# Kernel optimization log

Measured on AMD Instinct MI355X. Metric: run time of the kernel, lower is better.

## Reference

```python
import jax, jax.numpy as jnp
import numpy as np
from functools import partial

N = 10  # n_qubits (static)


def _rx(state, w, theta, n):
    # state: [B, 2^n] complex64; RX(theta) on wire w (wire 0 = most significant)
    B = state.shape[0]
    st = state.reshape(B, 2 ** w, 2, 2 ** (n - 1 - w))
    half = jnp.asarray(theta, state.real.dtype) * 0.5
    c = jnp.cos(half).reshape(-1, 1, 1)
    s = jnp.sin(half).reshape(-1, 1, 1)
    s0, s1 = st[:, :, 0], st[:, :, 1]
    n0 = c * s0 - 1j * s * s1
    n1 = -1j * s * s0 + c * s1
    return jnp.stack([n0, n1], axis=2).reshape(B, 2 ** n)


def _cnot(state, control, target, n):
    B = state.shape[0]
    a, bb = (control, target) if control < target else (target, control)
    st = state.reshape(B, 2 ** a, 2, 2 ** (bb - a - 1), 2, 2 ** (n - 1 - bb))
    if control == a:
        # control is axis 2, target axis 4: flip target where control==1
        c1 = jnp.flip(st[:, :, 1], axis=3)
        st = jnp.stack([st[:, :, 0], c1], axis=2)
    else:
        # control is axis 4, target axis 2: flip axis-2 slice where control==1
        c1 = jnp.flip(st[:, :, :, :, 1], axis=1)
        st = jnp.stack([st[:, :, :, :, 0], c1], axis=4)
    return st.reshape(B, 2 ** n)


def _expect_z(state, n):
    B = state.shape[0]
    probs = jnp.abs(state) ** 2  # [B, 2^n]
    es = []
    for w in range(n):
        p = probs.reshape(B, 2 ** w, 2, 2 ** (n - 1 - w))
        es.append(p[:, :, 0].sum((1, 2)) - p[:, :, 1].sum((1, 2)))
    return jnp.stack(es, axis=1)  # [B, n]


def _qlayer(x, theta, n):
    # x: [B, n] encoder angles; theta: [n] trainable RX angles
    B = x.shape[0]
    state = jnp.zeros((B, 2 ** n), jnp.complex64).at[:, 0].set(1.0)
    for w in range(n):
        state = _rx(state, w, x[:, w], n)
    for w in range(n):
        state = _rx(state, w, theta[w], n)
    for w in range(n - 1):
        state = _cnot(state, w, w + 1, n)
    state = _cnot(state, n - 1, 0, n)
    return _expect_z(state, n)


def setup_inputs() -> dict:
    key = jax.random.key(0)
    k1, k2, k3, k4 = jax.random.split(key, 4)
    T, B, D, H = 64, 256, 246, N
    inputs = jax.random.normal(k1, (T, B, D), jnp.float32)
    fan_in = D + H
    W = jax.random.normal(k2, (4, N, fan_in), jnp.float32) / np.sqrt(fan_in)
    b = jax.random.normal(k3, (4, N), jnp.float32) * 0.01
    thetas = jax.random.normal(k4, (4, N), jnp.float32)
    return {"inputs": inputs, "W": W, "b": b, "thetas": thetas}


def reference(inputs, W, b, thetas):
    T, B, D = inputs.shape
    H = thetas.shape[-1]
    qlayer4 = jax.vmap(partial(_qlayer, n=N))  # over the 4 gates

    def step(carry, x_t):
        hx, cx = carry
        comb = jnp.concatenate([x_t, hx], axis=1)          # [B, D+H]
        z = jnp.einsum('bi,goi->gbo', comb, W) + b[:, None, :]  # [4, B, n]
        gates = qlayer4(z, thetas)                          # [4, B, n]
        f = jax.nn.sigmoid(gates[0])
        i = jax.nn.sigmoid(gates[1])
        g = jnp.tanh(gates[2])
        o = jax.nn.sigmoid(gates[3])
        cx = f * cx + i * g
        hx = o * jnp.tanh(cx)
        return (hx, cx), hx

    hx0 = jnp.zeros((B, H), inputs.dtype)
    cx0 = jnp.zeros((B, H), inputs.dtype)
    (hx, cx), outputs = jax.lax.scan(step, (hx0, cx0), inputs)
    return outputs, hx, cx
```

## Files before the change

kernel.cpp:

```cpp
#include <hip/hip_runtime.h>
#include <hip/hip_bf16.h>

#define D_IN   246
#define NW     10
#define NG     4
#define NOUT   40
#define FANIN  256
#define BATCH  256
#define TSTEPS 64
#define NPAIR  123
#define WPK_ELEMS (NG * NPAIR * 20)

__global__ __launch_bounds__(256) void k_wt(const float* __restrict__ W,
                                            float* __restrict__ Wpk) {
    int e = blockIdx.x * 256 + threadIdx.x;
    if (e >= WPK_ELEMS) return;
    int q = e % 20;
    int j = (e / 20) % NPAIR;
    int g = e / (20 * NPAIR);
    int o = q >> 1, k = q & 1;
    Wpk[e] = W[(g * NW + o) * FANIN + (2 * j + k)];
}

__global__ __launch_bounds__(512) void k_gemm(
    const float* __restrict__ x,
    const float* __restrict__ Wpk,
    const float* __restrict__ bias,
    const float* __restrict__ theta,
    float* __restrict__ zxT)
{
    const int t    = blockIdx.x;
    const int bq   = blockIdx.y;
    const int tid  = threadIdx.x;
    const int lane = tid & 63;
    const int wv   = __builtin_amdgcn_readfirstlane(tid >> 6);
    const int g    = wv & 3;
    const int kh   = wv >> 2;

    __shared__ float xl[64 * D_IN];
    __shared__ float pr[NG][64][NW];

    const float* xsrc = x + ((size_t)t * BATCH + bq * 64) * D_IN;
    for (int k = tid; k < 64 * NPAIR; k += 512) {
        int row = k / NPAIR;
        int j   = k - row * NPAIR;
        float2 v = *reinterpret_cast<const float2*>(xsrc + row * D_IN + 2 * j);
        *reinterpret_cast<float2*>(xl + row * D_IN + 2 * j) = v;
    }
    __syncthreads();

    const int jstart = kh ? 62 : 0;
    const int npairs = kh ? 61 : 62;

    unsigned long long wa = (unsigned long long)(Wpk + (g * NPAIR + jstart) * 20);
    asm("" : "+v"(wa));
    const float* wbase = (const float*)wa;

    float acc[NW];
#pragma unroll
    for (int o = 0; o < NW; ++o) acc[o] = 0.f;

    const float* xr = xl + lane * D_IN + 2 * jstart;

#pragma unroll 4
    for (int jj = 0; jj < npairs; ++jj) {
        float2 xv = *reinterpret_cast<const float2*>(xr + 2 * jj);
        const float4* w4 = reinterpret_cast<const float4*>(wbase + jj * 20);
        float4 wa0 = w4[0], wb = w4[1], wc = w4[2], wd = w4[3], we = w4[4];
        acc[0] = fmaf(xv.x, wa0.x, fmaf(xv.y, wa0.y, acc[0]));
        acc[1] = fmaf(xv.x, wa0.z, fmaf(xv.y, wa0.w, acc[1]));
        acc[2] = fmaf(xv.x, wb.x,  fmaf(xv.y, wb.y,  acc[2]));
        acc[3] = fmaf(xv.x, wb.z,  fmaf(xv.y, wb.w,  acc[3]));
        acc[4] = fmaf(xv.x, wc.x,  fmaf(xv.y, wc.y,  acc[4]));
        acc[5] = fmaf(xv.x, wc.z,  fmaf(xv.y, wc.w,  acc[5]));
        acc[6] = fmaf(xv.x, wd.x,  fmaf(xv.y, wd.y,  acc[6]));
        acc[7] = fmaf(xv.x, wd.z,  fmaf(xv.y, wd.w,  acc[7]));
        acc[8] = fmaf(xv.x, we.x,  fmaf(xv.y, we.y,  acc[8]));
        acc[9] = fmaf(xv.x, we.z,  fmaf(xv.y, we.w,  acc[9]));
    }

    if (kh == 1) {
#pragma unroll
        for (int o = 0; o < NW; ++o) pr[g][lane][o] = acc[o];
    }
    __syncthreads();

    if (kh == 0) {
        const int b = bq * 64 + lane;
        float* zo = zxT + ((size_t)b * TSTEPS + t) * NOUT + g;
#pragma unroll
        for (int o = 0; o < NW; ++o) {
            float v = acc[o] + pr[g][lane][o] + bias[g * NW + o] + theta[g * NW + o];
            zo[o * NG] = v;
        }
    }
}

template <int CTRL>
__device__ __forceinline__ float dpp_shr_mul(float p) {
    int up = __builtin_amdgcn_update_dpp(__float_as_int(1.0f), __float_as_int(p),
                                         CTRL, 0xF, 0xF, false);
    return p * __int_as_float(up);
}

__global__ __launch_bounds__(64) void k_scan(
    const float* __restrict__ zxT,
    const float* __restrict__ W,
    float* __restrict__ out,
    float* __restrict__ hxout,
    float* __restrict__ cxout)
{
    const int b    = blockIdx.x;
    const int lane = threadIdx.x;
    const int o16  = lane & 15;
    const int oc   = (o16 < NW) ? o16 : 0;

    __shared__ float zl[TSTEPS * NOUT];

    {
        const float4* s4 = reinterpret_cast<const float4*>(zxT + (size_t)b * TSTEPS * NOUT);
        float4* d4 = reinterpret_cast<float4*>(zl);
#pragma unroll
        for (int q = 0; q < 10; ++q) d4[q * 64 + lane] = s4[q * 64 + lane];
    }

    float wh[NG][NW];
#pragma unroll
    for (int gg = 0; gg < NG; ++gg)
#pragma unroll
        for (int j = 0; j < NW; ++j)
            wh[gg][j] = W[(gg * NW + oc) * FANIN + D_IN + j];

    __syncthreads();

    float hx_s[NW];
#pragma unroll
    for (int j = 0; j < NW; ++j) hx_s[j] = 0.f;
    float cx = 0.f, hv = 0.f;

    const float* zrow = zl + oc * NG;
    float4 zn = *reinterpret_cast<const float4*>(zrow);
    float* outp = out + (size_t)b * NW + oc;

    for (int t = 0; t < TSTEPS; ++t) {
        float4 zc4 = zn;
        zn = *reinterpret_cast<const float4*>(zrow + ((t + 1) & 63) * NOUT);

        float z0 = zc4.x, z1 = zc4.y, z2 = zc4.z, z3 = zc4.w;
#pragma unroll
        for (int j = 0; j < NW; ++j) {
            z0 = fmaf(hx_s[j], wh[0][j], z0);
            z1 = fmaf(hx_s[j], wh[1][j], z1);
            z2 = fmaf(hx_s[j], wh[2][j], z2);
            z3 = fmaf(hx_s[j], wh[3][j], z3);
        }

        float p0 = __cosf(z0), p1 = __cosf(z1), p2 = __cosf(z2), p3 = __cosf(z3);

        p0 = dpp_shr_mul<0x111>(p0); p1 = dpp_shr_mul<0x111>(p1);
        p2 = dpp_shr_mul<0x111>(p2); p3 = dpp_shr_mul<0x111>(p3);
        p0 = dpp_shr_mul<0x112>(p0); p1 = dpp_shr_mul<0x112>(p1);
        p2 = dpp_shr_mul<0x112>(p2); p3 = dpp_shr_mul<0x112>(p3);
        p0 = dpp_shr_mul<0x114>(p0); p1 = dpp_shr_mul<0x114>(p1);
        p2 = dpp_shr_mul<0x114>(p2); p3 = dpp_shr_mul<0x114>(p3);
        p0 = dpp_shr_mul<0x118>(p0); p1 = dpp_shr_mul<0x118>(p1);
        p2 = dpp_shr_mul<0x118>(p2); p3 = dpp_shr_mul<0x118>(p3);

        float fg  = __fdividef(1.f, 1.f + __expf(-p0));
        float ig  = __fdividef(1.f, 1.f + __expf(-p1));
        float gg2 = 2.f * __fdividef(1.f, 1.f + __expf(-2.f * p2)) - 1.f;
        float og  = __fdividef(1.f, 1.f + __expf(-p3));

        cx = fmaf(fg, cx, ig * gg2);
        float e2 = __expf(cx + cx);
        float th = 1.f - __fdividef(2.f, 1.f + e2);
        hv = og * th;

        if (lane < NW) outp[(size_t)t * (BATCH * NW)] = hv;

#pragma unroll
        for (int j = 0; j < NW; ++j)
            hx_s[j] = __int_as_float(__builtin_amdgcn_readlane(__float_as_int(hv), j));
    }

    if (lane < NW) {
        hxout[b * NW + lane] = hv;
        cxout[b * NW + lane] = cx;
    }
}

extern "C" void kernel_launch(void* const* d_in, const int* in_sizes, int n_in,
                              void* d_out, int out_size, void* d_ws, size_t ws_size,
                              hipStream_t stream) {
    const float* x     = (const float*)d_in[0];
    const float* W     = (const float*)d_in[1];
    const float* bias  = (const float*)d_in[2];
    const float* theta = (const float*)d_in[3];

    float* out   = (float*)d_out;
    float* hxout = out + (size_t)TSTEPS * BATCH * NW;
    float* cxout = hxout + (size_t)BATCH * NW;

    float* Wpk = (float*)d_ws;
    float* zxT = Wpk + WPK_ELEMS;

    k_wt<<<(WPK_ELEMS + 255) / 256, 256, 0, stream>>>(W, Wpk);
    dim3 g1(TSTEPS, 4);
    k_gemm<<<g1, 512, 0, stream>>>(x, Wpk, bias, theta, zxT);
    k_scan<<<BATCH, 64, 0, stream>>>(zxT, W, out, hxout, cxout);
}
```

Baseline: 122.1 us.

## Fuse input projection GEMM into per-batch recurrent scan kernel

Merges the separate input-projection GEMM and the LSTM scan into one kernel with one 512-thread block per batch element. Each block computes all 64 timesteps of projections for its batch row in LDS, then wave 0 runs the recurrence. This removes the global zxT round trip and one kernel launch. In exchange, the 256 blocks read x rows strided across timesteps, and the remaining waves sit idle during the serial scan.

```diff
diff --git a/kernel.cpp b/kernel.cpp
--- a/kernel.cpp
+++ b/kernel.cpp
@@ -22,15 +22,24 @@
     Wpk[e] = W[(g * NW + o) * FANIN + (2 * j + k)];
 }
 
-__global__ __launch_bounds__(512) void k_gemm(
+template <int CTRL>
+__device__ __forceinline__ float dpp_shr_mul(float p) {
+    int up = __builtin_amdgcn_update_dpp(__float_as_int(1.0f), __float_as_int(p),
+                                         CTRL, 0xF, 0xF, false);
+    return p * __int_as_float(up);
+}
+
+__global__ __launch_bounds__(512) void k_fused(
     const float* __restrict__ x,
     const float* __restrict__ Wpk,
     const float* __restrict__ bias,
     const float* __restrict__ theta,
-    float* __restrict__ zxT)
+    const float* __restrict__ W,
+    float* __restrict__ out,
+    float* __restrict__ hxout,
+    float* __restrict__ cxout)
 {
-    const int t    = blockIdx.x;
-    const int bq   = blockIdx.y;
+    const int b    = blockIdx.x;
     const int tid  = threadIdx.x;
     const int lane = tid & 63;
     const int wv   = __builtin_amdgcn_readfirstlane(tid >> 6);
@@ -39,99 +48,76 @@
 
     __shared__ float xl[64 * D_IN];
     __shared__ float pr[NG][64][NW];
+    __shared__ float zl[TSTEPS * NOUT];
 
-    const float* xsrc = x + ((size_t)t * BATCH + bq * 64) * D_IN;
-    for (int k = tid; k < 64 * NPAIR; k += 512) {
-        int row = k / NPAIR;
-        int j   = k - row * NPAIR;
-        float2 v = *reinterpret_cast<const float2*>(xsrc + row * D_IN + 2 * j);
-        *reinterpret_cast<float2*>(xl + row * D_IN + 2 * j) = v;
+    const int o16 = lane & 15;
+    const int oc  = (o16 < NW) ? o16 : 0;
+    float wh[NG][NW];
+    if (wv == 0) {
+#pragma unroll
+        for (int gg = 0; gg < NG; ++gg)
+#pragma unroll
+            for (int j = 0; j < NW; ++j)
+                wh[gg][j] = W[(gg * NW + oc) * FANIN + D_IN + j];
+    }
+
+    for (int row = wv; row < 64; row += 8) {
+        const float* src = x + ((size_t)row * BATCH + b) * D_IN;
+        float* dst = xl + row * D_IN;
+        for (int j = lane; j < 123; j += 64) {
+            float2 v = *reinterpret_cast<const float2*>(src + 2 * j);
+            *reinterpret_cast<float2*>(dst + 2 * j) = v;
+        }
     }
     __syncthreads();
 
-    const int jstart = kh ? 62 : 0;
-    const int npairs = kh ? 61 : 62;
+    {
+        const int jstart = kh ? 62 : 0;
+        const int npairs = kh ? 61 : 62;
 
-    unsigned long long wa = (unsigned long long)(Wpk + (g * NPAIR + jstart) * 20);
-    asm("" : "+v"(wa));
-    const float* wbase = (const float*)wa;
+        unsigned long long wa = (unsigned long long)(Wpk + (g * NPAIR + jstart) * 20);
+        asm("" : "+v"(wa));
+        const float* wbase = (const float*)wa;
 
-    float acc[NW];
+        float acc[NW];
 #pragma unroll
-    for (int o = 0; o < NW; ++o) acc[o] = 0.f;
+        for (int o = 0; o < NW; ++o) acc[o] = 0.f;
 
-    const float* xr = xl + lane * D_IN + 2 * jstart;
+        const float* xr = xl + lane * D_IN + 2 * jstart;
 
 #pragma unroll 4
-    for (int jj = 0; jj < npairs; ++jj) {
-        float2 xv = *reinterpret_cast<const float2*>(xr + 2 * jj);
-        const float4* w4 = reinterpret_cast<const float4*>(wbase + jj * 20);
-        float4 wa0 = w4[0], wb = w4[1], wc = w4[2], wd = w4[3], we = w4[4];
-        acc[0] = fmaf(xv.x, wa0.x, fmaf(xv.y, wa0.y, acc[0]));
-        acc[1] = fmaf(xv.x, wa0.z, fmaf(xv.y, wa0.w, acc[1]));
-        acc[2] = fmaf(xv.x, wb.x,  fmaf(xv.y, wb.y,  acc[2]));
-        acc[3] = fmaf(xv.x, wb.z,  fmaf(xv.y, wb.w,  acc[3]));
-        acc[4] = fmaf(xv.x, wc.x,  fmaf(xv.y, wc.y,  acc[4]));
-        acc[5] = fmaf(xv.x, wc.z,  fmaf(xv.y, wc.w,  acc[5]));
-        acc[6] = fmaf(xv.x, wd.x,  fmaf(xv.y, wd.y,  acc[6]));
-        acc[7] = fmaf(xv.x, wd.z,  fmaf(xv.y, wd.w,  acc[7]));
-        acc[8] = fmaf(xv.x, we.x,  fmaf(xv.y, we.y,  acc[8]));
-        acc[9] = fmaf(xv.x, we.z,  fmaf(xv.y, we.w,  acc[9]));
-    }
+        for (int jj = 0; jj < npairs; ++jj) {
+            float2 xv = *reinterpret_cast<const float2*>(xr + 2 * jj);
+            const float4* w4 = reinterpret_cast<const float4*>(wbase + jj * 20);
+            float4 wa0 = w4[0], wb = w4[1], wc = w4[2], wd = w4[3], we = w4[4];
+            acc[0] = fmaf(xv.x, wa0.x, fmaf(xv.y, wa0.y, acc[0]));
+            acc[1] = fmaf(xv.x, wa0.z, fmaf(xv.y, wa0.w, acc[1]));
+            acc[2] = fmaf(xv.x, wb.x,  fmaf(xv.y, wb.y,  acc[2]));
+            acc[3] = fmaf(xv.x, wb.z,  fmaf(xv.y, wb.w,  acc[3]));
+            acc[4] = fmaf(xv.x, wc.x,  fmaf(xv.y, wc.y,  acc[4]));
+            acc[5] = fmaf(xv.x, wc.z,  fmaf(xv.y, wc.w,  acc[5]));
+            acc[6] = fmaf(xv.x, wd.x,  fmaf(xv.y, wd.y,  acc[6]));
+            acc[7] = fmaf(xv.x, wd.z,  fmaf(xv.y, wd.w,  acc[7]));
+            acc[8] = fmaf(xv.x, we.x,  fmaf(xv.y, we.y,  acc[8]));
+            acc[9] = fmaf(xv.x, we.z,  fmaf(xv.y, we.w,  acc[9]));
+        }
 
-    if (kh == 1) {
+        if (kh == 1) {
 #pragma unroll
-        for (int o = 0; o < NW; ++o) pr[g][lane][o] = acc[o];
+            for (int o = 0; o < NW; ++o) pr[g][lane][o] = acc[o];
+        }
+        __syncthreads();
+
+        if (kh == 0) {
+#pragma unroll
+            for (int o = 0; o < NW; ++o) {
+                float v = acc[o] + pr[g][lane][o] + bias[g * NW + o] + theta[g * NW + o];
+                zl[lane * NOUT + o * NG + g] = v;
+            }
+        }
     }
     __syncthreads();
-
-    if (kh == 0) {
-        const int b = bq * 64 + lane;
-        float* zo = zxT + ((size_t)b * TSTEPS + t) * NOUT + g;
-#pragma unroll
-        for (int o = 0; o < NW; ++o) {
-            float v = acc[o] + pr[g][lane][o] + bias[g * NW + o] + theta[g * NW + o];
-            zo[o * NG] = v;
-        }
-    }
-}
-
-template <int CTRL>
-__device__ __forceinline__ float dpp_shr_mul(float p) {
-    int up = __builtin_amdgcn_update_dpp(__float_as_int(1.0f), __float_as_int(p),
-                                         CTRL, 0xF, 0xF, false);
-    return p * __int_as_float(up);
-}
-
-__global__ __launch_bounds__(64) void k_scan(
-    const float* __restrict__ zxT,
-    const float* __restrict__ W,
-    float* __restrict__ out,
-    float* __restrict__ hxout,
-    float* __restrict__ cxout)
-{
-    const int b    = blockIdx.x;
-    const int lane = threadIdx.x;
-    const int o16  = lane & 15;
-    const int oc   = (o16 < NW) ? o16 : 0;
-
-    __shared__ float zl[TSTEPS * NOUT];
-
-    {
-        const float4* s4 = reinterpret_cast<const float4*>(zxT + (size_t)b * TSTEPS * NOUT);
-        float4* d4 = reinterpret_cast<float4*>(zl);
-#pragma unroll
-        for (int q = 0; q < 10; ++q) d4[q * 64 + lane] = s4[q * 64 + lane];
-    }
-
-    float wh[NG][NW];
-#pragma unroll
-    for (int gg = 0; gg < NG; ++gg)
-#pragma unroll
-        for (int j = 0; j < NW; ++j)
-            wh[gg][j] = W[(gg * NW + oc) * FANIN + D_IN + j];
-
-    __syncthreads();
+    if (wv != 0) return;
 
     float hx_s[NW];
 #pragma unroll
@@ -202,10 +188,7 @@
     float* cxout = hxout + (size_t)BATCH * NW;
 
     float* Wpk = (float*)d_ws;
-    float* zxT = Wpk + WPK_ELEMS;
 
     k_wt<<<(WPK_ELEMS + 255) / 256, 256, 0, stream>>>(W, Wpk);
-    dim3 g1(TSTEPS, 4);
-    k_gemm<<<g1, 512, 0, stream>>>(x, Wpk, bias, theta, zxT);
-    k_scan<<<BATCH, 64, 0, stream>>>(zxT, W, out, hxout, cxout);
+    k_fused<<<BATCH, 512, 0, stream>>>(x, Wpk, bias, theta, W, out, hxout, cxout);
 }
```

New measurement: 120.9 us. No clear change (-1.0%).
